# Kernel optimization log

Measured on AMD Instinct MI355X. Metric: run time of the kernel, lower is better.

## Reference

```python
import jax, jax.numpy as jnp
import numpy as np
from jax import lax

B, T, N, NS = 64, 32, 12, 132
ER, NR, EE, NE, ATTN = 256, 256, 128, 128, 64
K_NEIGH = NS // N  # 11 spatial edges per source node
TEMP = K_NEIGH / float(np.sqrt(ATTN))  # num_keys / sqrt(attn_size)
# src-major edge ordering: edges for node n as source are contiguous
NODE_TO_EDGES = jnp.arange(NS).reshape(N, K_NEIGH)


def _lstm_cell(x, h, c, Wih, Whh, bih, bhh):
    # torch.nn.LSTMCell gate order: i, f, g, o
    gates = x @ Wih.T + h @ Whh.T + bih + bhh
    i, f, g, o = jnp.split(gates, 4, axis=-1)
    c2 = jax.nn.sigmoid(f) * c + jax.nn.sigmoid(i) * jnp.tanh(g)
    h2 = jax.nn.sigmoid(o) * jnp.tanh(c2)
    return h2, c2


def _forward(nodes, edges_temporal, edges_spatial,
             W_te, b_te, te_Wih, te_Whh, te_bih, te_bhh,
             W_se, b_se, se_Wih, se_Whh, se_bih, se_bhh,
             Wq, bq, Wk, bk,
             W_node, b_node, W_edge, b_edge,
             nr_Wih, nr_Whh, nr_bih, nr_bhh,
             W_out, b_out):
    Bv = nodes.shape[0]
    dt = nodes.dtype

    def step(carry, xs):
        h_temp, c_temp, h_spat, c_spat, h_node, c_node = carry
        node_t, et, es = xs
        # temporal edge branch (dropout is identity at inference)
        te = jax.nn.relu(et @ W_te.T + b_te)                       # (B,N,EE)
        h_temp, c_temp = _lstm_cell(te, h_temp, c_temp, te_Wih, te_Whh, te_bih, te_bhh)
        # spatial edge branch
        se = jax.nn.relu(es @ W_se.T + b_se)                       # (B,NS,EE)
        h_spat, c_spat = _lstm_cell(se, h_spat, c_spat, se_Wih, se_Whh, se_bih, se_bhh)
        # attention over each node's 11 spatial edges
        q = h_temp @ Wq.T + bq                                     # (B,N,ATTN)
        hpn = h_spat[:, NODE_TO_EDGES]                             # (B,N,11,ER) gather
        k = hpn @ Wk.T + bk                                        # (B,N,11,ATTN)
        scores = jnp.einsum('bna,bnka->bnk', q, k)
        w = jax.nn.softmax(scores * TEMP, axis=-1)
        h_attn = jnp.einsum('bnk,bnke->bne', w, hpn)               # (B,N,ER)
        # node RNN
        nin = jax.nn.relu(node_t @ W_node.T + b_node)              # (B,N,NE)
        ein = jax.nn.relu(jnp.concatenate([h_temp, h_attn], -1) @ W_edge.T + b_edge)
        rin = jnp.concatenate([nin, ein], -1)                      # (B,N,2*NE)
        h_node, c_node = _lstm_cell(rin, h_node, c_node, nr_Wih, nr_Whh, nr_bih, nr_bhh)
        out = h_node @ W_out.T + b_out                             # (B,N,5)
        return (h_temp, c_temp, h_spat, c_spat, h_node, c_node), out

    z = lambda *s: jnp.zeros(s, dtype=dt)
    carry0 = (z(Bv, N, ER), z(Bv, N, ER), z(Bv, NS, ER), z(Bv, NS, ER), z(Bv, N, NR), z(Bv, N, NR))
    xs = (jnp.moveaxis(nodes, 1, 0), jnp.moveaxis(edges_temporal, 1, 0), jnp.moveaxis(edges_spatial, 1, 0))
    _, outs = lax.scan(step, carry0, xs)                           # (T,B,N,5)
    return jnp.moveaxis(outs, 0, 1)                                # (B,T,N,5)


def setup_inputs() -> dict:
    key = jax.random.key(0)
    ks = iter(jax.random.split(key, 40))
    def p(*shape):
        return jax.random.normal(next(ks), shape, dtype=jnp.float32) * 0.05
    return {
        'nodes': jax.random.normal(next(ks), (B, T, N, 2), dtype=jnp.float32),
        'edges_temporal': jax.random.normal(next(ks), (B, T, N, 2), dtype=jnp.float32),
        'edges_spatial': jax.random.normal(next(ks), (B, T, NS, 2), dtype=jnp.float32),
        'W_te': p(EE, 2), 'b_te': p(EE),
        'te_Wih': p(4 * ER, EE), 'te_Whh': p(4 * ER, ER), 'te_bih': p(4 * ER), 'te_bhh': p(4 * ER),
        'W_se': p(EE, 2), 'b_se': p(EE),
        'se_Wih': p(4 * ER, EE), 'se_Whh': p(4 * ER, ER), 'se_bih': p(4 * ER), 'se_bhh': p(4 * ER),
        'Wq': p(ATTN, ER), 'bq': p(ATTN), 'Wk': p(ATTN, ER), 'bk': p(ATTN),
        'W_node': p(NE, 2), 'b_node': p(NE),
        'W_edge': p(NE, 2 * ER), 'b_edge': p(NE),
        'nr_Wih': p(4 * NR, 2 * NE), 'nr_Whh': p(4 * NR, NR), 'nr_bih': p(4 * NR), 'nr_bhh': p(4 * NR),
        'W_out': p(5, NR), 'b_out': p(5),
    }


def reference(nodes, edges_temporal, edges_spatial,
              W_te, b_te, te_Wih, te_Whh, te_bih, te_bhh,
              W_se, b_se, se_Wih, se_Whh, se_bih, se_bhh,
              Wq, bq, Wk, bk,
              W_node, b_node, W_edge, b_edge,
              nr_Wih, nr_Whh, nr_bih, nr_bhh,
              W_out, b_out):
    return _forward(nodes, edges_temporal, edges_spatial,
                    W_te, b_te, te_Wih, te_Whh, te_bih, te_bhh,
                    W_se, b_se, se_Wih, se_Whh, se_bih, se_bhh,
                    Wq, bq, Wk, bk,
                    W_node, b_node, W_edge, b_edge,
                    nr_Wih, nr_Whh, nr_bih, nr_bhh,
                    W_out, b_out)
```

## Files before the change

kernel.cpp:

```cpp
#include <hip/hip_runtime.h>
#include <math.h>

#define B_ 64
#define T_ 32
#define N_ 12
#define NS_ 132
#define KN_ 11
#define TEMP_ 1.375f

typedef unsigned short u16;
typedef __attribute__((ext_vector_type(8))) short bf16x8;
typedef __attribute__((ext_vector_type(8))) unsigned short u16x8;
typedef __attribute__((ext_vector_type(4))) float f32x4;

__device__ __forceinline__ float sigm(float x) { return 1.f / (1.f + __expf(-x)); }
__device__ __forceinline__ float ftanh(float x) {
    float a = fabsf(x);
    float e = __expf(-2.f * a);
    float t = (1.f - e) / (1.f + e);
    return copysignf(t, x);
}
__device__ __forceinline__ u16 f2bf(float x) {
    union { float f; unsigned u; } v; v.f = x;
    unsigned r = v.u + 0x7fffu + ((v.u >> 16) & 1u);
    return (u16)(r >> 16);
}
__device__ __forceinline__ float bf2f(u16 h) {
    union { unsigned u; float f; } v; v.u = ((unsigned)h) << 16; return v.f;
}
__device__ __forceinline__ int origcol(int j) {
    return ((j >> 4) & 3) * 256 + ((j >> 6) << 4) + (j & 15);
}

__device__ __forceinline__ const u16* frag_row8(const u16* basef, int row, int k, int nkc) {
    return basef + (((size_t)(row >> 4) * nkc + (k >> 5)) * 512)
                 + ((((k >> 3) & 3) * 16 + (row & 15)) * 8);
}

__global__ __launch_bounds__(256) void prep_kernel(
    const float* __restrict__ te_Wih, const float* __restrict__ te_Whh,
    const float* __restrict__ te_bih, const float* __restrict__ te_bhh,
    const float* __restrict__ se_Wih, const float* __restrict__ se_Whh,
    const float* __restrict__ se_bih, const float* __restrict__ se_bhh,
    const float* __restrict__ nr_Wih, const float* __restrict__ nr_Whh,
    const float* __restrict__ nr_bih, const float* __restrict__ nr_bhh,
    const float* __restrict__ Wq, const float* __restrict__ Wk,
    const float* __restrict__ W_edge,
    u16* __restrict__ Wf_t, u16* __restrict__ Wf_s, u16* __restrict__ Wf_n,
    float* __restrict__ bs_t, float* __restrict__ bs_s, float* __restrict__ bs_n,
    u16* __restrict__ Wqf, u16* __restrict__ Wkqf, u16* __restrict__ Wef)
{
    int idx = blockIdx.x * 256 + threadIdx.x;
    if (idx < 49152) {
        int l = idx & 63, kc = (idx >> 6) % 12, jb16 = idx / 768;
        int j = jb16 * 16 + (l & 15);
        int c = origcol(j);
        int k0 = kc * 32 + (l >> 4) * 8;
        u16x8 vt, vs;
        #pragma unroll
        for (int i = 0; i < 8; ++i) {
            int k = k0 + i;
            vt[i] = f2bf((k < 128) ? te_Wih[c * 128 + k] : te_Whh[c * 256 + (k - 128)]);
            vs[i] = f2bf((k < 128) ? se_Wih[c * 128 + k] : se_Whh[c * 256 + (k - 128)]);
        }
        *(u16x8*)(Wf_t + (size_t)idx * 8) = vt;
        *(u16x8*)(Wf_s + (size_t)idx * 8) = vs;
    }
    if (idx < 65536) {
        int l = idx & 63, kc = (idx >> 6) & 15, jb16 = idx >> 10;
        int j = jb16 * 16 + (l & 15);
        int c = origcol(j);
        int k0 = kc * 32 + (l >> 4) * 8;
        u16x8 vn;
        #pragma unroll
        for (int i = 0; i < 8; ++i) {
            int k = k0 + i;
            vn[i] = f2bf((k < 256) ? nr_Wih[c * 256 + k] : nr_Whh[c * 256 + (k - 256)]);
        }
        *(u16x8*)(Wf_n + (size_t)idx * 8) = vn;
    }
    if (idx < 1024) {
        int c = origcol(idx);
        bs_t[idx] = te_bih[c] + te_bhh[c];
        bs_s[idx] = se_bih[c] + se_bhh[c];
        bs_n[idx] = nr_bih[c] + nr_bhh[c];
    }
    if (idx < 2048) {
        int l = idx & 63, tile = idx >> 6;
        int a = (tile >> 3) * 16 + (l & 15);
        int k0 = (tile & 7) * 32 + (l >> 4) * 8;
        u16x8 v;
        #pragma unroll
        for (int i = 0; i < 8; ++i) v[i] = f2bf(Wq[a * 256 + k0 + i]);
        *(u16x8*)(Wqf + (size_t)idx * 8) = v;
    }
    if (idx < 2048) {
        int l = idx & 63, tile = idx >> 6;
        int j = (tile >> 1) * 16 + (l & 15);
        int a0 = (tile & 1) * 32 + (l >> 4) * 8;
        u16x8 v;
        #pragma unroll
        for (int i = 0; i < 8; ++i) v[i] = f2bf(Wk[(a0 + i) * 256 + j]);
        *(u16x8*)(Wkqf + (size_t)idx * 8) = v;
    }
    if (idx < 8192) {
        int l = idx & 63, tile = idx >> 6;
        int c = (tile >> 4) * 16 + (l & 15);
        int k0 = (tile & 15) * 32 + (l >> 4) * 8;
        u16x8 v;
        #pragma unroll
        for (int i = 0; i < 8; ++i) v[i] = f2bf(W_edge[c * 512 + k0 + i]);
        *(u16x8*)(Wef + (size_t)idx * 8) = v;
    }
}

__global__ __launch_bounds__(256) void emb_nin_kernel(
    const float* __restrict__ nodes,
    const float* __restrict__ W_node, const float* __restrict__ b_node,
    u16* __restrict__ ninf)
{
    int u = blockIdx.x * 256 + threadIdx.x;
    int l = u & 63, kc = (u >> 6) & 3;
    int rt = u >> 8;
    int rb16 = rt % 48, t = rt / 48;
    int row = rb16 * 16 + (l & 15);
    int b = row / 12, n = row - b * 12;
    size_t src = (((size_t)b * T_ + t) * N_ + n) * 2;
    float n0 = nodes[src], n1 = nodes[src + 1];
    int k0 = kc * 32 + (l >> 4) * 8;
    u16x8 vn;
    #pragma unroll
    for (int i = 0; i < 8; ++i) {
        int k = k0 + i;
        float y = fmaf(n0, W_node[k * 2], fmaf(n1, W_node[k * 2 + 1], b_node[k]));
        vn[i] = f2bf(fmaxf(y, 0.f));
    }
    *(u16x8*)(ninf + (size_t)u * 8) = vn;
}

__global__ __launch_bounds__(256) void step_kernel(
    int nA, int nN, int iL,
    const float* __restrict__ es, const float* __restrict__ et,
    const float* __restrict__ W_se, const float* __restrict__ b_se,
    const float* __restrict__ W_te, const float* __restrict__ b_te,
    const u16* __restrict__ Wf_t, const float* __restrict__ bs_t,
    const u16* __restrict__ Wf_s, const float* __restrict__ bs_s,
    const u16* __restrict__ L_htp, u16* __restrict__ L_htc, float* __restrict__ c_t,
    const u16* __restrict__ L_hsp, u16* __restrict__ L_hsc, float* __restrict__ c_s,
    const u16* __restrict__ A_htf, const u16* __restrict__ A_hsf,
    u16* __restrict__ A_ein,
    const u16* __restrict__ Wqf, const float* __restrict__ bq,
    const u16* __restrict__ Wkqf, const float* __restrict__ bk,
    const u16* __restrict__ Wef, const float* __restrict__ b_edge,
    const u16* __restrict__ ninf_m, const u16* __restrict__ N_ein,
    const u16* __restrict__ Wf_n, const float* __restrict__ bs_n,
    const u16* __restrict__ N_hnp, u16* __restrict__ N_hnc,
    u16* __restrict__ hist1, float* __restrict__ c_n)
{
    const int tid = threadIdx.x;
    const int l = tid & 63, l15 = l & 15;
    const size_t lo8 = (size_t)l * 8;
    const int wid = tid >> 6;

    if ((int)blockIdx.x >= nA + nN) {
        const int lb = blockIdx.x - nA - nN;
        const bool spatial = lb < 528;
        int rb, jc;
        if (spatial) { int orig = (lb & 7) * 66 + (lb >> 3); rb = orig >> 3; jc = orig & 7; }
        else         { int q = lb - 528;                      rb = q >> 3;    jc = q & 7; }
        const int ns = spatial ? NS_ : N_;
        const float* E    = spatial ? es : et;
        const float* Wemb = spatial ? W_se : W_te;
        const float* bemb = spatial ? b_se : b_te;
        const u16* Wf     = spatial ? Wf_s : Wf_t;
        const float* bs   = spatial ? bs_s : bs_t;
        const u16* Hf = spatial ? L_hsp : L_htp;
        u16*       Hc = spatial ? L_hsc : L_htc;
        float* C  = spatial ? c_s : c_t;

        const int wm = wid >> 1, wn = wid & 1;
        const int rb16 = rb * 8 + wm * 4;
        const int jb16 = jc * 8 + wn * 4;
        const int kemb0 = (l >> 4) * 8;

        float biasv[4];
        #pragma unroll
        for (int g = 0; g < 4; ++g) biasv[g] = bs[jc * 128 + wn * 64 + g * 16 + l15];

        float e0[4], e1[4];
        #pragma unroll
        for (int mf = 0; mf < 4; ++mf) {
            int row = (rb16 + mf) * 16 + l15;
            int b = row / ns, s = row - b * ns;
            const float* ep = E + (((size_t)b * T_ + iL) * ns + s) * 2;
            e0[mf] = ep[0]; e1[mf] = ep[1];
        }

        f32x4 acc[4][4];
        #pragma unroll
        for (int mf = 0; mf < 4; ++mf)
            #pragma unroll
            for (int g = 0; g < 4; ++g)
                acc[mf][g] = (f32x4){biasv[g], biasv[g], biasv[g], biasv[g]};

        #pragma unroll
        for (int kc = 0; kc < 12; ++kc) {
            bf16x8 a[4], b[4];
            if (kc < 4) {
                #pragma unroll
                for (int mf = 0; mf < 4; ++mf) {
                    u16x8 v;
                    #pragma unroll
                    for (int e = 0; e < 8; ++e) {
                        int k = kc * 32 + kemb0 + e;
                        float x = fmaf(e0[mf], Wemb[k * 2],
                                  fmaf(e1[mf], Wemb[k * 2 + 1], bemb[k]));
                        v[e] = f2bf(fmaxf(x, 0.f));
                    }
                    a[mf] = (bf16x8)v;
                }
            } else {
                #pragma unroll
                for (int mf = 0; mf < 4; ++mf)
                    a[mf] = *(const bf16x8*)(Hf + (((size_t)(rb16 + mf)) * 8 + (kc - 4)) * 512 + lo8);
            }
            #pragma unroll
            for (int g = 0; g < 4; ++g)
                b[g] = *(const bf16x8*)(Wf + (((size_t)(jb16 + g)) * 12 + kc) * 512 + lo8);
            #pragma unroll
            for (int mf = 0; mf < 4; ++mf)
                #pragma unroll
                for (int g = 0; g < 4; ++g)
                    acc[mf][g] = __builtin_amdgcn_mfma_f32_16x16x32_bf16(a[mf], b[g], acc[mf][g], 0, 0, 0);
        }

        const int cell = (jc * 2 + wn) * 16 + l15;
        const int rofs = (l >> 4) << 2;
        const int cpart = (cell >> 5) * 512 + ((cell >> 3) & 3) * 128 + (cell & 7);
        #pragma unroll
        for (int mf = 0; mf < 4; ++mf) {
            int r16 = rb16 + mf;
            #pragma unroll
            for (int r = 0; r < 4; ++r) {
                int rlow = rofs + r;
                size_t doff = ((size_t)r16 * 16 + rlow) * 256 + cell;
                float gi = acc[mf][0][r], gf = acc[mf][1][r];
                float gg = acc[mf][2][r], go = acc[mf][3][r];
                float c2 = sigm(gf) * C[doff] + sigm(gi) * ftanh(gg);
                float h2 = sigm(go) * ftanh(c2);
                C[doff] = c2;
                Hc[(size_t)r16 * 4096 + cpart + rlow * 8] = f2bf(h2);
            }
        }
        return;
    }

    if ((int)blockIdx.x >= nA) {
        const int nb = blockIdx.x - nA;
        const int rb16 = nb >> 2, jq = nb & 3;
        const int wn = wid;

        f32x4 acc[4];
        #pragma unroll
        for (int g = 0; g < 4; ++g) {
            float bv = bs_n[jq * 256 + wn * 64 + g * 16 + l15];
            acc[g] = (f32x4){bv, bv, bv, bv};
        }
        #pragma unroll
        for (int kc = 0; kc < 16; ++kc) {
            const u16* p;
            if (kc < 4)       p = ninf_m + ((size_t)rb16 * 4 + kc) * 512 + lo8;
            else if (kc < 8)  p = N_ein  + ((size_t)rb16 * 4 + (kc - 4)) * 512 + lo8;
            else              p = N_hnp  + ((size_t)rb16 * 8 + (kc - 8)) * 512 + lo8;
            bf16x8 af = *(const bf16x8*)p;
            #pragma unroll
            for (int g = 0; g < 4; ++g) {
                bf16x8 bf = *(const bf16x8*)(Wf_n + (((size_t)(jq * 16 + wn * 4 + g)) * 16 + kc) * 512 + lo8);
                acc[g] = __builtin_amdgcn_mfma_f32_16x16x32_bf16(af, bf, acc[g], 0, 0, 0);
            }
        }
        const int cell = (jq * 4 + wn) * 16 + l15;
        const int rofs = (l >> 4) << 2;
        const int cpart = (cell >> 5) * 512 + ((cell >> 3) & 3) * 128 + (cell & 7);
        #pragma unroll
        for (int r = 0; r < 4; ++r) {
            int rlow = rofs + r;
            size_t doff = ((size_t)rb16 * 16 + rlow) * 256 + cell;
            float gi = acc[0][r], gf = acc[1][r], gg = acc[2][r], go = acc[3][r];
            float c2 = sigm(gf) * c_n[doff] + sigm(gi) * ftanh(gg);
            float h2 = sigm(go) * ftanh(c2);
            c_n[doff] = c2;
            u16 hb = f2bf(h2);
            hist1[doff] = hb;
            N_hnc[(size_t)rb16 * 4096 + cpart + rlow * 8] = hb;
        }
        return;
    }

    const int rb16n = blockIdx.x;

    __shared__ float q_lds[16][68];
    __shared__ float shbuf[16][260];
    __shared__ float sc_lds[16][12];
    __shared__ float w_lds[16][12];
    __shared__ float qb_lds[16];

    {
        f32x4 qa = (f32x4){0.f, 0.f, 0.f, 0.f};
        #pragma unroll
        for (int kc = 0; kc < 8; ++kc) {
            bf16x8 af = *(const bf16x8*)(A_htf + ((size_t)rb16n * 8 + kc) * 512 + lo8);
            bf16x8 bf = *(const bf16x8*)(Wqf + ((size_t)(wid * 8 + kc)) * 512 + lo8);
            qa = __builtin_amdgcn_mfma_f32_16x16x32_bf16(af, bf, qa, 0, 0, 0);
        }
        int a = wid * 16 + l15;
        #pragma unroll
        for (int r = 0; r < 4; ++r)
            q_lds[(l >> 4) * 4 + r][a] = qa[r] + bq[a];
    }
    __syncthreads();
    {
        f32x4 ka[4];
        #pragma unroll
        for (int j2 = 0; j2 < 4; ++j2) ka[j2] = (f32x4){0.f, 0.f, 0.f, 0.f};
        #pragma unroll
        for (int kc = 0; kc < 2; ++kc) {
            int a0 = kc * 32 + (l >> 4) * 8;
            bf16x8 af;
            #pragma unroll
            for (int e = 0; e < 8; ++e)
                ((u16*)&af)[e] = f2bf(q_lds[l15][a0 + e]);
            #pragma unroll
            for (int j2 = 0; j2 < 4; ++j2) {
                bf16x8 bf = *(const bf16x8*)(Wkqf + ((size_t)((wid * 4 + j2) * 2 + kc)) * 512 + lo8);
                ka[j2] = __builtin_amdgcn_mfma_f32_16x16x32_bf16(af, bf, ka[j2], 0, 0, 0);
            }
        }
        #pragma unroll
        for (int j2 = 0; j2 < 4; ++j2)
            #pragma unroll
            for (int r = 0; r < 4; ++r)
                shbuf[(l >> 4) * 4 + r][(wid * 4 + j2) * 16 + l15] = ka[j2][r];
        if (tid < 16) {
            float s = 0.f;
            for (int a = 0; a < 64; ++a) s = fmaf(q_lds[tid][a], bk[a], s);
            qb_lds[tid] = s;
        }
    }
    __syncthreads();
    if (tid < 176) {
        int row = tid / 11, kk = tid - row * 11;
        int r = rb16n * 16 + row;
        int srow = (r / 12) * 132 + (r % 12) * 11 + kk;
        float s = 0.f;
        #pragma unroll
        for (int k = 0; k < 256; k += 8) {
            u16x8 v = *(const u16x8*)frag_row8(A_hsf, srow, k, 8);
            #pragma unroll
            for (int e = 0; e < 8; ++e) s = fmaf(shbuf[row][k + e], bf2f(v[e]), s);
        }
        sc_lds[row][kk] = (s + qb_lds[row]) * TEMP_;
    }
    __syncthreads();
    if (tid < 16) {
        float m = sc_lds[tid][0];
        #pragma unroll
        for (int kk = 1; kk < 11; ++kk) m = fmaxf(m, sc_lds[tid][kk]);
        float ssum = 0.f;
        float wv[11];
        #pragma unroll
        for (int kk = 0; kk < 11; ++kk) { wv[kk] = __expf(sc_lds[tid][kk] - m); ssum += wv[kk]; }
        float inv = 1.f / ssum;
        #pragma unroll
        for (int kk = 0; kk < 11; ++kk) w_lds[tid][kk] = wv[kk] * inv;
    }
    __syncthreads();
    {
        int row = tid >> 4, c0 = (tid & 15) * 16;
        int r = rb16n * 16 + row;
        int sbase = (r / 12) * 132 + (r % 12) * 11;
        float hacc[16];
        #pragma unroll
        for (int e = 0; e < 16; ++e) hacc[e] = 0.f;
        #pragma unroll
        for (int kk = 0; kk < 11; ++kk) {
            float wv = w_lds[row][kk];
            int srow = sbase + kk;
            u16x8 v0 = *(const u16x8*)frag_row8(A_hsf, srow, c0, 8);
            u16x8 v1 = *(const u16x8*)frag_row8(A_hsf, srow, c0 + 8, 8);
            #pragma unroll
            for (int e = 0; e < 8; ++e) {
                hacc[e]     = fmaf(wv, bf2f(v0[e]), hacc[e]);
                hacc[8 + e] = fmaf(wv, bf2f(v1[e]), hacc[8 + e]);
            }
        }
        #pragma unroll
        for (int e = 0; e < 16; ++e) shbuf[row][c0 + e] = hacc[e];
    }
    __syncthreads();
    {
        f32x4 ea[2];
        ea[0] = (f32x4){0.f, 0.f, 0.f, 0.f};
        ea[1] = (f32x4){0.f, 0.f, 0.f, 0.f};
        #pragma unroll
        for (int kc = 0; kc < 16; ++kc) {
            bf16x8 af;
            if (kc < 8) {
                af = *(const bf16x8*)(A_htf + ((size_t)rb16n * 8 + kc) * 512 + lo8);
            } else {
                int k0 = (kc - 8) * 32 + (l >> 4) * 8;
                #pragma unroll
                for (int e = 0; e < 8; ++e)
                    ((u16*)&af)[e] = f2bf(shbuf[l15][k0 + e]);
            }
            #pragma unroll
            for (int j2 = 0; j2 < 2; ++j2) {
                bf16x8 bf = *(const bf16x8*)(Wef + ((size_t)((wid * 2 + j2) * 16 + kc)) * 512 + lo8);
                ea[j2] = __builtin_amdgcn_mfma_f32_16x16x32_bf16(af, bf, ea[j2], 0, 0, 0);
            }
        }
        #pragma unroll
        for (int j2 = 0; j2 < 2; ++j2) {
            int cell = (wid * 2 + j2) * 16 + l15;
            #pragma unroll
            for (int r = 0; r < 4; ++r) {
                int row = (l >> 4) * 4 + r;
                float v = ea[j2][r] + b_edge[cell];
                v = v > 0.f ? v : 0.f;
                A_ein[((size_t)rb16n * 4 + (cell >> 5)) * 512
                      + (((cell >> 3) & 3) * 16 + row) * 8 + (cell & 7)] = f2bf(v);
            }
        }
    }
}

__global__ __launch_bounds__(256) void out_kernel(
    const u16* __restrict__ hist1, const float* __restrict__ W_out,
    const float* __restrict__ b_out, float* __restrict__ out)
{
    const int lane = threadIdx.x & 63;
    const int grp = threadIdx.x >> 6;
    for (int ridx = blockIdx.x * 4 + grp; ridx < 32 * 768; ridx += gridDim.x * 4) {
        int t = ridx / 768, row = ridx % 768;
        int b = row / 12, n = row % 12;
        const u16* h = &hist1[(size_t)ridx * 256];
        float hv[4];
        #pragma unroll
        for (int i = 0; i < 4; ++i) hv[i] = bf2f(h[i * 64 + lane]);
        #pragma unroll
        for (int q = 0; q < 5; ++q) {
            float s = 0.f;
            #pragma unroll
            for (int i = 0; i < 4; ++i) s = fmaf(hv[i], W_out[q * 256 + i * 64 + lane], s);
            #pragma unroll
            for (int off = 32; off > 0; off >>= 1) s += __shfl_down(s, off, 64);
            if (lane == 0)
                out[(((size_t)b * T_ + t) * N_ + n) * 5 + q] = s + b_out[q];
        }
    }
}

extern "C" void kernel_launch(void* const* d_in, const int* in_sizes, int n_in,
                              void* d_out, int out_size, void* d_ws, size_t ws_size,
                              hipStream_t stream)
{
    const float* nodes = (const float*)d_in[0];
    const float* et    = (const float*)d_in[1];
    const float* es    = (const float*)d_in[2];
    const float* W_te = (const float*)d_in[3];  const float* b_te = (const float*)d_in[4];
    const float* te_Wih = (const float*)d_in[5]; const float* te_Whh = (const float*)d_in[6];
    const float* te_bih = (const float*)d_in[7]; const float* te_bhh = (const float*)d_in[8];
    const float* W_se = (const float*)d_in[9];  const float* b_se = (const float*)d_in[10];
    const float* se_Wih = (const float*)d_in[11]; const float* se_Whh = (const float*)d_in[12];
    const float* se_bih = (const float*)d_in[13]; const float* se_bhh = (const float*)d_in[14];
    const float* Wq = (const float*)d_in[15]; const float* bq = (const float*)d_in[16];
    const float* Wk = (const float*)d_in[17]; const float* bk = (const float*)d_in[18];
    const float* W_node = (const float*)d_in[19]; const float* b_node = (const float*)d_in[20];
    const float* W_edge = (const float*)d_in[21]; const float* b_edge = (const float*)d_in[22];
    const float* nr_Wih = (const float*)d_in[23]; const float* nr_Whh = (const float*)d_in[24];
    const float* nr_bih = (const float*)d_in[25]; const float* nr_bhh = (const float*)d_in[26];
    const float* W_out = (const float*)d_in[27]; const float* b_out = (const float*)d_in[28];

    char* base = (char*)d_ws;
    size_t off = 0;
    auto A = [&](size_t bytes) { char* p = base + off; off += (bytes + 255) & ~(size_t)255; return p; };

    float* c_t = (float*)A(768 * 256 * 4);
    float* c_s = (float*)A((size_t)8448 * 256 * 4);
    float* c_n = (float*)A(768 * 256 * 4);
    u16* htf0 = (u16*)A(768 * 256 * 2);
    u16* hsf0 = (u16*)A((size_t)8448 * 256 * 2);
    u16* hnf0 = (u16*)A(768 * 256 * 2);
    size_t zero_bytes = off;
    u16* htf1 = (u16*)A(768 * 256 * 2);
    u16* hsf1 = (u16*)A((size_t)8448 * 256 * 2);
    u16* hnf1 = (u16*)A(768 * 256 * 2);
    u16* einf0 = (u16*)A(768 * 128 * 2);
    u16* einf1 = (u16*)A(768 * 128 * 2);
    u16* hist = (u16*)A((size_t)33 * 768 * 256 * 2);
    u16* ninf = (u16*)A((size_t)32 * 768 * 128 * 2);
    u16* Wf_t = (u16*)A(1024 * 384 * 2);
    u16* Wf_s = (u16*)A(1024 * 384 * 2);
    u16* Wf_n = (u16*)A(1024 * 512 * 2);
    float* bs_t = (float*)A(1024 * 4);
    float* bs_s = (float*)A(1024 * 4);
    float* bs_n = (float*)A(1024 * 4);
    u16* Wqf  = (u16*)A(2048 * 8 * 2);
    u16* Wkqf = (u16*)A(2048 * 8 * 2);
    u16* Wef  = (u16*)A(8192 * 8 * 2);
    (void)ws_size;

    hipMemsetAsync(base, 0, zero_bytes, stream);

    prep_kernel<<<256, 256, 0, stream>>>(
        te_Wih, te_Whh, te_bih, te_bhh, se_Wih, se_Whh, se_bih, se_bhh,
        nr_Wih, nr_Whh, nr_bih, nr_bhh, Wq, Wk, W_edge,
        Wf_t, Wf_s, Wf_n, bs_t, bs_s, bs_n, Wqf, Wkqf, Wef);

    emb_nin_kernel<<<1536, 256, 0, stream>>>(nodes, W_node, b_node, ninf);

    u16* htf[2] = {htf0, htf1};
    u16* hsf[2] = {hsf0, hsf1};
    u16* hnf[2] = {hnf0, hnf1};
    u16* einf[2] = {einf0, einf1};

    step_kernel<<<576, 256, 0, stream>>>(
        0, 0, 0,
        es, et, W_se, b_se, W_te, b_te,
        Wf_t, bs_t, Wf_s, bs_s,
        htf[0], htf[1], c_t,
        hsf[0], hsf[1], c_s,
        htf[0], hsf[0], einf[0],
        Wqf, bq, Wkqf, bk, Wef, b_edge,
        ninf, einf[0], Wf_n, bs_n, hnf[0], hnf[1], hist, c_n);

    for (int t = 0; t < T_; ++t) {
        int nN = (t >= 1) ? 192 : 0;
        int nL = (t < T_ - 1) ? 576 : 0;
        int s = t + 1;
        int m = (t >= 1) ? (t - 1) : 0;
        step_kernel<<<48 + nN + nL, 256, 0, stream>>>(
            48, nN, s,
            es, et, W_se, b_se, W_te, b_te,
            Wf_t, bs_t, Wf_s, bs_s,
            htf[s & 1], htf[(s + 1) & 1], c_t,
            hsf[s & 1], hsf[(s + 1) & 1], c_s,
            htf[(t + 1) & 1], hsf[(t + 1) & 1], einf[t & 1],
            Wqf, bq, Wkqf, bk, Wef, b_edge,
            ninf + (size_t)m * 48 * 4 * 512, einf[m & 1], Wf_n, bs_n,
            hnf[m & 1], hnf[(m + 1) & 1], hist + (size_t)(m + 1) * 768 * 256, c_n);
    }

    {
        int m = T_ - 1;
        step_kernel<<<192, 256, 0, stream>>>(
            0, 192, 0,
            es, et, W_se, b_se, W_te, b_te,
            Wf_t, bs_t, Wf_s, bs_s,
            htf[0], htf[1], c_t,
            hsf[0], hsf[1], c_s,
            htf[0], hsf[0], einf[0],
            Wqf, bq, Wkqf, bk, Wef, b_edge,
            ninf + (size_t)m * 48 * 4 * 512, einf[m & 1], Wf_n, bs_n,
            hnf[m & 1], hnf[(m + 1) & 1], hist + (size_t)(m + 1) * 768 * 256, c_n);
    }

    out_kernel<<<1536, 256, 0, stream>>>(hist + (size_t)768 * 256, W_out, b_out, (float*)d_out);
}
```

Before: 1.068 ms.

## Fold Wq and Wk into a precomputed matrix for attention scores

```diff
diff --git a/kernel.cpp b/kernel.cpp
--- a/kernel.cpp
+++ b/kernel.cpp
@@ -44,11 +44,13 @@
     const float* __restrict__ se_bih, const float* __restrict__ se_bhh,
     const float* __restrict__ nr_Wih, const float* __restrict__ nr_Whh,
     const float* __restrict__ nr_bih, const float* __restrict__ nr_bhh,
-    const float* __restrict__ Wq, const float* __restrict__ Wk,
+    const float* __restrict__ Wq, const float* __restrict__ bq,
+    const float* __restrict__ Wk, const float* __restrict__ bk,
     const float* __restrict__ W_edge,
     u16* __restrict__ Wf_t, u16* __restrict__ Wf_s, u16* __restrict__ Wf_n,
     float* __restrict__ bs_t, float* __restrict__ bs_s, float* __restrict__ bs_n,
-    u16* __restrict__ Wqf, u16* __restrict__ Wkqf, u16* __restrict__ Wef)
+    u16* __restrict__ Mf, float* __restrict__ c0v, float* __restrict__ vqb,
+    float* __restrict__ s0v, u16* __restrict__ Wef)
 {
     int idx = blockIdx.x * 256 + threadIdx.x;
     if (idx < 49152) {
@@ -85,23 +87,38 @@
         bs_s[idx] = se_bih[c] + se_bhh[c];
         bs_n[idx] = nr_bih[c] + nr_bhh[c];
     }
-    if (idx < 2048) {
+    if (idx < 8192) {
         int l = idx & 63, tile = idx >> 6;
-        int a = (tile >> 3) * 16 + (l & 15);
-        int k0 = (tile & 7) * 32 + (l >> 4) * 8;
+        int jb = tile >> 3, kc = tile & 7;
+        int j = jb * 16 + (l & 15);
+        int k0 = kc * 32 + (l >> 4) * 8;
+        float m[8];
+        #pragma unroll
+        for (int e = 0; e < 8; ++e) m[e] = 0.f;
+        for (int a = 0; a < 64; ++a) {
+            float wk = Wk[a * 256 + j];
+            const float* wq = Wq + a * 256 + k0;
+            #pragma unroll
+            for (int e = 0; e < 8; ++e) m[e] = fmaf(wk, wq[e], m[e]);
+        }
         u16x8 v;
         #pragma unroll
-        for (int i = 0; i < 8; ++i) v[i] = f2bf(Wq[a * 256 + k0 + i]);
-        *(u16x8*)(Wqf + (size_t)idx * 8) = v;
-    }
-    if (idx < 2048) {
-        int l = idx & 63, tile = idx >> 6;
-        int j = (tile >> 1) * 16 + (l & 15);
-        int a0 = (tile & 1) * 32 + (l >> 4) * 8;
-        u16x8 v;
-        #pragma unroll
-        for (int i = 0; i < 8; ++i) v[i] = f2bf(Wk[(a0 + i) * 256 + j]);
-        *(u16x8*)(Wkqf + (size_t)idx * 8) = v;
+        for (int e = 0; e < 8; ++e) v[e] = f2bf(m[e]);
+        *(u16x8*)(Mf + (size_t)idx * 8) = v;
+    }
+    if (idx < 256) {
+        float s = 0.f, s2 = 0.f;
+        for (int a = 0; a < 64; ++a) {
+            s  = fmaf(Wk[a * 256 + idx], bq[a], s);
+            s2 = fmaf(Wq[a * 256 + idx], bk[a], s2);
+        }
+        c0v[idx] = s;
+        vqb[idx] = s2;
+        if (idx == 0) {
+            float s3 = 0.f;
+            for (int a = 0; a < 64; ++a) s3 = fmaf(bq[a], bk[a], s3);
+            s0v[0] = s3;
+        }
     }
     if (idx < 8192) {
         int l = idx & 63, tile = idx >> 6;
@@ -149,8 +166,8 @@
     const u16* __restrict__ L_hsp, u16* __restrict__ L_hsc, float* __restrict__ c_s,
     const u16* __restrict__ A_htf, const u16* __restrict__ A_hsf,
     u16* __restrict__ A_ein,
-    const u16* __restrict__ Wqf, const float* __restrict__ bq,
-    const u16* __restrict__ Wkqf, const float* __restrict__ bk,
+    const u16* __restrict__ Mf, const float* __restrict__ c0v,
+    const float* __restrict__ vqb, const float* __restrict__ s0v,
     const u16* __restrict__ Wef, const float* __restrict__ b_edge,
     const u16* __restrict__ ninf_m, const u16* __restrict__ N_ein,
     const u16* __restrict__ Wf_n, const float* __restrict__ bs_n,
@@ -299,53 +316,44 @@
 
     const int rb16n = blockIdx.x;
 
-    __shared__ float q_lds[16][68];
     __shared__ float shbuf[16][260];
+    __shared__ float qbp[16][16];
     __shared__ float sc_lds[16][12];
     __shared__ float w_lds[16][12];
-    __shared__ float qb_lds[16];
 
     {
-        f32x4 qa = (f32x4){0.f, 0.f, 0.f, 0.f};
+        f32x4 ka[4];
+        #pragma unroll
+        for (int j2 = 0; j2 < 4; ++j2) ka[j2] = (f32x4){0.f, 0.f, 0.f, 0.f};
         #pragma unroll
         for (int kc = 0; kc < 8; ++kc) {
             bf16x8 af = *(const bf16x8*)(A_htf + ((size_t)rb16n * 8 + kc) * 512 + lo8);
-            bf16x8 bf = *(const bf16x8*)(Wqf + ((size_t)(wid * 8 + kc)) * 512 + lo8);
-            qa = __builtin_amdgcn_mfma_f32_16x16x32_bf16(af, bf, qa, 0, 0, 0);
-        }
-        int a = wid * 16 + l15;
-        #pragma unroll
-        for (int r = 0; r < 4; ++r)
-            q_lds[(l >> 4) * 4 + r][a] = qa[r] + bq[a];
-    }
-    __syncthreads();
+            #pragma unroll
+            for (int j2 = 0; j2 < 4; ++j2) {
+                bf16x8 bf = *(const bf16x8*)(Mf + ((size_t)((wid * 4 + j2) * 8 + kc)) * 512 + lo8);
+                ka[j2] = __builtin_amdgcn_mfma_f32_16x16x32_bf16(af, bf, ka[j2], 0, 0, 0);
+            }
+        }
+        #pragma unroll
+        for (int j2 = 0; j2 < 4; ++j2) {
+            int j = (wid * 4 + j2) * 16 + l15;
+            #pragma unroll
+            for (int r = 0; r < 4; ++r)
+                shbuf[(l >> 4) * 4 + r][j] = ka[j2][r] + c0v[j];
+        }
+    }
     {
-        f32x4 ka[4];
-        #pragma unroll
-        for (int j2 = 0; j2 < 4; ++j2) ka[j2] = (f32x4){0.f, 0.f, 0.f, 0.f};
-        #pragma unroll
-        for (int kc = 0; kc < 2; ++kc) {
-            int a0 = kc * 32 + (l >> 4) * 8;
-            bf16x8 af;
-            #pragma unroll
-            for (int e = 0; e < 8; ++e)
-                ((u16*)&af)[e] = f2bf(q_lds[l15][a0 + e]);
-            #pragma unroll
-            for (int j2 = 0; j2 < 4; ++j2) {
-                bf16x8 bf = *(const bf16x8*)(Wkqf + ((size_t)((wid * 4 + j2) * 2 + kc)) * 512 + lo8);
-                ka[j2] = __builtin_amdgcn_mfma_f32_16x16x32_bf16(af, bf, ka[j2], 0, 0, 0);
-            }
-        }
-        #pragma unroll
-        for (int j2 = 0; j2 < 4; ++j2)
-            #pragma unroll
-            for (int r = 0; r < 4; ++r)
-                shbuf[(l >> 4) * 4 + r][(wid * 4 + j2) * 16 + l15] = ka[j2][r];
-        if (tid < 16) {
-            float s = 0.f;
-            for (int a = 0; a < 64; ++a) s = fmaf(q_lds[tid][a], bk[a], s);
-            qb_lds[tid] = s;
-        }
+        int row = tid >> 4, kc16 = tid & 15;
+        int r = rb16n * 16 + row;
+        u16x8 v0 = *(const u16x8*)frag_row8(A_htf, r, kc16 * 16, 8);
+        u16x8 v1 = *(const u16x8*)frag_row8(A_htf, r, kc16 * 16 + 8, 8);
+        float s = 0.f;
+        #pragma unroll
+        for (int e = 0; e < 8; ++e) {
+            s = fmaf(bf2f(v0[e]), vqb[kc16 * 16 + e], s);
+            s = fmaf(bf2f(v1[e]), vqb[kc16 * 16 + 8 + e], s);
+        }
+        qbp[row][kc16] = s;
     }
     __syncthreads();
     if (tid < 176) {
@@ -359,7 +367,10 @@
             #pragma unroll
             for (int e = 0; e < 8; ++e) s = fmaf(shbuf[row][k + e], bf2f(v[e]), s);
         }
-        sc_lds[row][kk] = (s + qb_lds[row]) * TEMP_;
+        float qb = s0v[0];
+        #pragma unroll
+        for (int p = 0; p < 16; ++p) qb += qbp[row][p];
+        sc_lds[row][kk] = (s + qb) * TEMP_;
     }
     __syncthreads();
     if (tid < 16) {
@@ -505,8 +516,10 @@
     float* bs_t = (float*)A(1024 * 4);
     float* bs_s = (float*)A(1024 * 4);
     float* bs_n = (float*)A(1024 * 4);
-    u16* Wqf  = (u16*)A(2048 * 8 * 2);
-    u16* Wkqf = (u16*)A(2048 * 8 * 2);
+    u16* Mf   = (u16*)A(8192 * 8 * 2);
+    float* c0v = (float*)A(256 * 4);
+    float* vqb = (float*)A(256 * 4);
+    float* s0v = (float*)A(256);
     u16* Wef  = (u16*)A(8192 * 8 * 2);
     (void)ws_size;
 
@@ -514,8 +527,8 @@
 
     prep_kernel<<<256, 256, 0, stream>>>(
         te_Wih, te_Whh, te_bih, te_bhh, se_Wih, se_Whh, se_bih, se_bhh,
-        nr_Wih, nr_Whh, nr_bih, nr_bhh, Wq, Wk, W_edge,
-        Wf_t, Wf_s, Wf_n, bs_t, bs_s, bs_n, Wqf, Wkqf, Wef);
+        nr_Wih, nr_Whh, nr_bih, nr_bhh, Wq, bq, Wk, bk, W_edge,
+        Wf_t, Wf_s, Wf_n, bs_t, bs_s, bs_n, Mf, c0v, vqb, s0v, Wef);
 
     emb_nin_kernel<<<1536, 256, 0, stream>>>(nodes, W_node, b_node, ninf);
 
@@ -531,7 +544,7 @@
         htf[0], htf[1], c_t,
         hsf[0], hsf[1], c_s,
         htf[0], hsf[0], einf[0],
-        Wqf, bq, Wkqf, bk, Wef, b_edge,
+        Mf, c0v, vqb, s0v, Wef, b_edge,
         ninf, einf[0], Wf_n, bs_n, hnf[0], hnf[1], hist, c_n);
 
     for (int t = 0; t < T_; ++t) {
@@ -546,7 +559,7 @@
             htf[s & 1], htf[(s + 1) & 1], c_t,
             hsf[s & 1], hsf[(s + 1) & 1], c_s,
             htf[(t + 1) & 1], hsf[(t + 1) & 1], einf[t & 1],
-            Wqf, bq, Wkqf, bk, Wef, b_edge,
+            Mf, c0v, vqb, s0v, Wef, b_edge,
             ninf + (size_t)m * 48 * 4 * 512, einf[m & 1], Wf_n, bs_n,
             hnf[m & 1], hnf[(m + 1) & 1], hist + (size_t)(m + 1) * 768 * 256, c_n);
     }
@@ -560,7 +573,7 @@
             htf[0], htf[1], c_t,
             hsf[0], hsf[1], c_s,
             htf[0], hsf[0], einf[0],
-            Wqf, bq, Wkqf, bk, Wef, b_edge,
+            Mf, c0v, vqb, s0v, Wef, b_edge,
             ninf + (size_t)m * 48 * 4 * 512, einf[m & 1], Wf_n, bs_n,
             hnf[m & 1], hnf[(m + 1) & 1], hist + (size_t)(m + 1) * 768 * 256, c_n);
     }
```

After: 1.610 ms. 1.51x slower.
